# Kernel optimization log

Hardware: AMD Instinct MI355X
Metric: run time of the kernel (lower is better)

## Reference

```python
import jax, jax.numpy as jnp
import numpy as np

B, T, C = 32, 2048, 1024  # batch, seq_len (<= block_size), n_embd
HEAD_SIZE = 128


def setup_inputs() -> dict:
    key = jax.random.key(0)
    kx, kk, kq, kv = jax.random.split(key, 4)
    std = 0.02  # CustomLinear init: normal(0, 0.02)
    return {
        "x": jax.random.normal(kx, (B, T, C), dtype=jnp.float32),
        "Wk": jax.random.normal(kk, (HEAD_SIZE, C), dtype=jnp.float32) * std,
        "Wq": jax.random.normal(kq, (HEAD_SIZE, C), dtype=jnp.float32) * std,
        "Wv": jax.random.normal(kv, (HEAD_SIZE, C), dtype=jnp.float32) * std,
    }


def reference(x, Wk, Wq, Wv):
    # x: [B, T, C]; W*: [head_size, C] (torch Linear layout, no bias)
    Bb, Tt, Cc = x.shape
    k = jnp.einsum("btc,hc->bth", x, Wk)
    q = jnp.einsum("btc,hc->bth", x, Wq)
    v = jnp.einsum("btc,hc->bth", x, Wv)
    # NOTE: original scales by C**-0.5 (n_embd), not head_size**-0.5
    wei = jnp.einsum("bth,bsh->bts", q, k) * (Cc ** -0.5)
    causal = jnp.tril(jnp.ones((Tt, Tt), dtype=bool))  # tril[:T,:T]
    wei = jnp.where(causal, wei, -jnp.inf)
    wei = jax.nn.softmax(wei, axis=-1)
    return jnp.einsum("bts,bsh->bth", wei, v)  # [B, T, head_size]
```

## Files before the change

### kernel.cpp

```cpp
#include <hip/hip_runtime.h>
#include <hip/hip_bf16.h>

typedef __bf16 bf8_t __attribute__((ext_vector_type(8)));
typedef __bf16 bf4_t __attribute__((ext_vector_type(4)));
typedef float f4_t __attribute__((ext_vector_type(4)));

#define B_ 32
#define T_ 2048
#define C_ 1024
#define H_ 128

__global__ __launch_bounds__(256) void wconv_kernel(
    const float* __restrict__ Wk, const float* __restrict__ Wq, const float* __restrict__ Wv,
    __bf16* __restrict__ Wr)
{
    const int e  = (blockIdx.x * 256 + threadIdx.x) * 8;
    const int kk = e & 31;
    const int lr = (e >> 5) & 15;
    const int ks = (e >> 9) & 31;
    const int cg = e >> 14;
    const int col = cg * 16 + lr;
    const int k   = ks * 32 + kk;
    const float* W = (col < 128) ? Wk : (col < 256) ? Wq : Wv;
    const float* p = W + (size_t)(col & 127) * C_ + k;
    float4 f0 = *(const float4*)p;
    float4 f1 = *(const float4*)(p + 4);
    bf8_t o;
    o[0] = (__bf16)f0.x; o[1] = (__bf16)f0.y; o[2] = (__bf16)f0.z; o[3] = (__bf16)f0.w;
    o[4] = (__bf16)f1.x; o[5] = (__bf16)f1.y; o[6] = (__bf16)f1.z; o[7] = (__bf16)f1.w;
    *(bf8_t*)(Wr + e) = o;
}

__global__ __launch_bounds__(256, 1) void proj_kernel(
    const float* __restrict__ x, const __bf16* __restrict__ Wr,
    __bf16* __restrict__ Kb, __bf16* __restrict__ Qb, __bf16* __restrict__ VtG)
{
    __shared__ __bf16 Xs[64][C_ + 8];

    const int m0   = blockIdx.x * 64;
    const int tid  = threadIdx.x;
    const int lane = tid & 63;
    const int wn   = tid >> 6;
    const int lr   = lane & 15;
    const int quad = lane >> 4;
    const int r0   = tid >> 4;
    const int kc   = (tid & 15) << 3;

    f4_t acc[4][6];
    #pragma unroll
    for (int mi = 0; mi < 4; mi++)
        #pragma unroll
        for (int ni = 0; ni < 6; ni++) acc[mi][ni] = f4_t{0.f, 0.f, 0.f, 0.f};

    float4 bufA[8], bufB[8];

#define LOADC(buf, c) { _Pragma("unroll") \
    for (int i_ = 0; i_ < 4; ++i_) { \
        const float* p_ = x + (size_t)(m0 + r0 + i_ * 16) * C_ + (c) * 128 + kc; \
        buf[2 * i_]     = *(const float4*)p_; \
        buf[2 * i_ + 1] = *(const float4*)(p_ + 4); } }

#define WRITEC(buf, c) { _Pragma("unroll") \
    for (int i_ = 0; i_ < 4; ++i_) { \
        float4 a_ = buf[2 * i_], b_ = buf[2 * i_ + 1]; \
        bf8_t o_; \
        o_[0] = (__bf16)a_.x; o_[1] = (__bf16)a_.y; o_[2] = (__bf16)a_.z; o_[3] = (__bf16)a_.w; \
        o_[4] = (__bf16)b_.x; o_[5] = (__bf16)b_.y; o_[6] = (__bf16)b_.z; o_[7] = (__bf16)b_.w; \
        *(bf8_t*)&Xs[r0 + i_ * 16][(c) * 128 + kc] = o_; } }

#define COMPUTE(c) { _Pragma("unroll") \
    for (int k4_ = 0; k4_ < 4; ++k4_) { \
        const int ks_ = (c) * 4 + k4_; \
        bf8_t xa_[4]; \
        _Pragma("unroll") \
        for (int mi = 0; mi < 4; ++mi) \
            xa_[mi] = *(const bf8_t*)&Xs[mi * 16 + lr][ks_ * 32 + quad * 8]; \
        _Pragma("unroll") \
        for (int ni = 0; ni < 6; ++ni) { \
            bf8_t wb_ = *(const bf8_t*)(Wr + (size_t)((ni * 4 + wn) * 32 + ks_) * 512 + lr * 32 + quad * 8); \
            if (ni < 4) { \
                _Pragma("unroll") \
                for (int mi = 0; mi < 4; ++mi) \
                    acc[mi][ni] = __builtin_amdgcn_mfma_f32_16x16x32_bf16(xa_[mi], wb_, acc[mi][ni], 0, 0, 0); \
            } else { \
                _Pragma("unroll") \
                for (int mi = 0; mi < 4; ++mi) \
                    acc[mi][ni] = __builtin_amdgcn_mfma_f32_16x16x32_bf16(wb_, xa_[mi], acc[mi][ni], 0, 0, 0); \
            } } } }

    LOADC(bufA, 0)
    LOADC(bufB, 1)
    WRITEC(bufA, 0)
    __syncthreads();

    #pragma unroll
    for (int c = 0; c < 8; ++c) {
        if (c < 6) { if (c & 1) LOADC(bufB, c + 2) else LOADC(bufA, c + 2) }
        COMPUTE(c)
        if (c < 7) {
            if (c & 1) WRITEC(bufA, c + 1) else WRITEC(bufB, c + 1)
            __syncthreads();
        }
    }

#undef LOADC
#undef WRITEC
#undef COMPUTE

    const int bb = m0 >> 11;
    const int t0 = m0 & (T_ - 1);
    #pragma unroll
    for (int ni = 0; ni < 4; ni++) {
        __bf16* Out = (ni < 2) ? Kb : Qb;
        const int col = (ni & 1) * 64 + wn * 16 + lr;
        #pragma unroll
        for (int mi = 0; mi < 4; mi++)
            for (int r = 0; r < 4; r++) {
                const int row = m0 + mi * 16 + quad * 4 + r;
                Out[(size_t)row * H_ + col] = (__bf16)acc[mi][ni][r];
            }
    }
    #pragma unroll
    for (int ni = 4; ni < 6; ni++)
        for (int mi = 0; mi < 4; mi++) {
            const int tok = t0 + mi * 16 + lr;
            #pragma unroll
            for (int r = 0; r < 4; r++) {
                const int h = (ni - 4) * 64 + wn * 16 + quad * 4 + r;
                VtG[(size_t)bb * H_ * T_ + (size_t)h * T_ + tok] = (__bf16)acc[mi][ni][r];
            }
        }
}

__global__ __launch_bounds__(512, 4) void flash_kernel(
    const __bf16* __restrict__ Qb, const __bf16* __restrict__ Kb,
    const __bf16* __restrict__ VtG, float* __restrict__ Out)
{
    __shared__ __bf16 Ks[64][136];
    __shared__ __bf16 Vt[128][72];
    __shared__ __bf16 Ps[128][72];

    const int qt = (blockIdx.y < 16) ? (15 - blockIdx.x) : blockIdx.x;
    const int b  = blockIdx.y;
    const size_t kqbase = (size_t)b * T_ * H_;
    const size_t vbase  = (size_t)b * H_ * T_;

    const int tid  = threadIdx.x;
    const int lane = tid & 63;
    const int w    = tid >> 6;
    const int lr   = lane & 15;
    const int quad = lane >> 4;

    bf8_t qf[4];
    {
        const __bf16* qp = Qb + kqbase + (size_t)(qt * 128 + w * 16 + lr) * H_ + quad * 8;
        #pragma unroll
        for (int ks = 0; ks < 4; ks++) qf[ks] = *(const bf8_t*)(qp + ks * 32);
    }

    f4_t o[8];
    #pragma unroll
    for (int n = 0; n < 8; n++) o[n] = f4_t{0.f, 0.f, 0.f, 0.f};
    float ls[4] = {0.f, 0.f, 0.f, 0.f};

    const float sc = 0.03125f * 1.4426950408889634f;
    const int jmax = 2 * qt + 1;

    const int kRow0 = tid >> 4,          kC0 = (tid & 15) << 3;
    const int kRow1 = (tid + 512) >> 4,  kC1 = ((tid + 512) & 15) << 3;
    const int vH0 = tid >> 3,            vS0 = (tid & 7) << 3;
    const int vH1 = (tid + 512) >> 3,    vS1 = ((tid + 512) & 7) << 3;

    bf8_t kr0 = *(const bf8_t*)(Kb + kqbase + (size_t)kRow0 * H_ + kC0);
    bf8_t kr1 = *(const bf8_t*)(Kb + kqbase + (size_t)kRow1 * H_ + kC1);
    bf8_t vr0 = *(const bf8_t*)(VtG + vbase + (size_t)vH0 * T_ + vS0);
    bf8_t vr1 = *(const bf8_t*)(VtG + vbase + (size_t)vH1 * T_ + vS1);

    for (int j = 0; j <= jmax; j++) {
        __syncthreads();
        *(bf8_t*)&Ks[kRow0][kC0] = kr0;
        *(bf8_t*)&Ks[kRow1][kC1] = kr1;
        *(bf8_t*)&Vt[vH0][vS0]   = vr0;
        *(bf8_t*)&Vt[vH1][vS1]   = vr1;
        __syncthreads();
        if (j < jmax) {
            const int s0 = (j + 1) * 64;
            kr0 = *(const bf8_t*)(Kb + kqbase + (size_t)(s0 + kRow0) * H_ + kC0);
            kr1 = *(const bf8_t*)(Kb + kqbase + (size_t)(s0 + kRow1) * H_ + kC1);
            vr0 = *(const bf8_t*)(VtG + vbase + (size_t)vH0 * T_ + s0 + vS0);
            vr1 = *(const bf8_t*)(VtG + vbase + (size_t)vH1 * T_ + s0 + vS1);
        }
        if (j == jmax && w < 4) continue;

        f4_t s4[4];
        #pragma unroll
        for (int n = 0; n < 4; n++) s4[n] = f4_t{0.f, 0.f, 0.f, 0.f};
        #pragma unroll
        for (int ks = 0; ks < 4; ks++)
            for (int n = 0; n < 4; n++) {
                bf8_t kf = *(const bf8_t*)&Ks[n * 16 + lr][ks * 32 + quad * 8];
                s4[n] = __builtin_amdgcn_mfma_f32_16x16x32_bf16(qf[ks], kf, s4[n], 0, 0, 0);
            }

        const bool domask = (j - 2 * qt) == (w >> 2);
        const int rowg = qt * 128 + w * 16 + quad * 4;
        #pragma unroll
        for (int n = 0; n < 4; n++) {
            const int colg = j * 64 + n * 16 + lr;
            #pragma unroll
            for (int r = 0; r < 4; r++) {
                float p = __builtin_exp2f(s4[n][r] * sc);
                if (domask && colg > rowg + r) p = 0.f;
                ls[r] += p;
                Ps[w * 16 + quad * 4 + r][n * 16 + lr] = (__bf16)p;
            }
        }

        #pragma unroll
        for (int ks = 0; ks < 2; ks++) {
            bf8_t pf = *(const bf8_t*)&Ps[w * 16 + lr][ks * 32 + quad * 8];
            #pragma unroll
            for (int n = 0; n < 8; n++) {
                bf8_t vf = *(const bf8_t*)&Vt[n * 16 + lr][ks * 32 + quad * 8];
                o[n] = __builtin_amdgcn_mfma_f32_16x16x32_bf16(pf, vf, o[n], 0, 0, 0);
            }
        }
    }

    float inv[4];
    #pragma unroll
    for (int r = 0; r < 4; r++) {
        float v = ls[r];
        v += __shfl_xor(v, 1);
        v += __shfl_xor(v, 2);
        v += __shfl_xor(v, 4);
        v += __shfl_xor(v, 8);
        inv[r] = 1.f / v;
    }
    #pragma unroll
    for (int n = 0; n < 8; n++) {
        const int col = n * 16 + lr;
        #pragma unroll
        for (int r = 0; r < 4; r++) {
            const int row = qt * 128 + w * 16 + quad * 4 + r;
            Out[kqbase + (size_t)row * H_ + col] = o[n][r] * inv[r];
        }
    }
}

extern "C" void kernel_launch(void* const* d_in, const int* in_sizes, int n_in,
                              void* d_out, int out_size, void* d_ws, size_t ws_size,
                              hipStream_t stream) {
    const float* x  = (const float*)d_in[0];
    const float* Wk = (const float*)d_in[1];
    const float* Wq = (const float*)d_in[2];
    const float* Wv = (const float*)d_in[3];
    float* out = (float*)d_out;

    const size_t n_kqv = (size_t)B_ * T_ * H_;
    __bf16* Kb  = (__bf16*)d_ws;
    __bf16* Qb  = Kb + n_kqv;
    __bf16* VtG = Qb + n_kqv;
    __bf16* Wr  = VtG + n_kqv;

    wconv_kernel<<<dim3(192), 256, 0, stream>>>(Wk, Wq, Wv, Wr);
    proj_kernel<<<dim3((B_ * T_) / 64), 256, 0, stream>>>(x, Wr, Kb, Qb, VtG);
    flash_kernel<<<dim3(16, B_), 512, 0, stream>>>(Qb, Kb, VtG, out);
}
```

Baseline: 518.5 us.

## Shrink projection LDS tile to double-buffered 128-wide chunks, use 8 waves per block

The projection kernel used to stage a full 64x1024 bf16 tile of x in shared memory (about 130 KB), which allowed only one block per CU. It now double-buffers 64x128 chunks (about 35 KB) and uses 512 threads, with the waves split 2x4 over rows and columns. Each wave holds half the accumulators, and launch bounds are raised to allow 4 blocks per CU. The aim is higher occupancy and better latency hiding for the x loads. In exchange, each Wr fragment is loaded by twice as many waves, and the prefetch is only one chunk ahead.

```diff
diff --git a/kernel.cpp b/kernel.cpp
--- a/kernel.cpp
+++ b/kernel.cpp
@@ -31,74 +31,71 @@
     *(bf8_t*)(Wr + e) = o;
 }
 
-__global__ __launch_bounds__(256, 1) void proj_kernel(
+__global__ __launch_bounds__(512, 4) void proj_kernel(
     const float* __restrict__ x, const __bf16* __restrict__ Wr,
     __bf16* __restrict__ Kb, __bf16* __restrict__ Qb, __bf16* __restrict__ VtG)
 {
-    __shared__ __bf16 Xs[64][C_ + 8];
+    __shared__ __bf16 Xs[2][64][136];
 
     const int m0   = blockIdx.x * 64;
     const int tid  = threadIdx.x;
     const int lane = tid & 63;
-    const int wn   = tid >> 6;
+    const int w    = tid >> 6;
+    const int wm   = w >> 2;
+    const int wn   = w & 3;
     const int lr   = lane & 15;
     const int quad = lane >> 4;
-    const int r0   = tid >> 4;
-    const int kc   = (tid & 15) << 3;
-
-    f4_t acc[4][6];
-    #pragma unroll
-    for (int mi = 0; mi < 4; mi++)
+
+    const int r0 = tid >> 5;
+    const int c4 = (tid & 31) << 2;
+
+    f4_t acc[2][6];
+    #pragma unroll
+    for (int mi = 0; mi < 2; mi++)
         #pragma unroll
         for (int ni = 0; ni < 6; ni++) acc[mi][ni] = f4_t{0.f, 0.f, 0.f, 0.f};
 
-    float4 bufA[8], bufB[8];
-
-#define LOADC(buf, c) { _Pragma("unroll") \
+    float4 pf[4];
+
+#define LOADC(c) { _Pragma("unroll") \
+    for (int i_ = 0; i_ < 4; ++i_) \
+        pf[i_] = *(const float4*)(x + (size_t)(m0 + r0 + i_ * 16) * C_ + (c) * 128 + c4); }
+
+#define WRITEC(bsel) { _Pragma("unroll") \
     for (int i_ = 0; i_ < 4; ++i_) { \
-        const float* p_ = x + (size_t)(m0 + r0 + i_ * 16) * C_ + (c) * 128 + kc; \
-        buf[2 * i_]     = *(const float4*)p_; \
-        buf[2 * i_ + 1] = *(const float4*)(p_ + 4); } }
-
-#define WRITEC(buf, c) { _Pragma("unroll") \
-    for (int i_ = 0; i_ < 4; ++i_) { \
-        float4 a_ = buf[2 * i_], b_ = buf[2 * i_ + 1]; \
-        bf8_t o_; \
-        o_[0] = (__bf16)a_.x; o_[1] = (__bf16)a_.y; o_[2] = (__bf16)a_.z; o_[3] = (__bf16)a_.w; \
-        o_[4] = (__bf16)b_.x; o_[5] = (__bf16)b_.y; o_[6] = (__bf16)b_.z; o_[7] = (__bf16)b_.w; \
-        *(bf8_t*)&Xs[r0 + i_ * 16][(c) * 128 + kc] = o_; } }
-
-#define COMPUTE(c) { _Pragma("unroll") \
+        float4 f_ = pf[i_]; \
+        *(bf4_t*)&Xs[bsel][r0 + i_ * 16][c4] = \
+            bf4_t{(__bf16)f_.x, (__bf16)f_.y, (__bf16)f_.z, (__bf16)f_.w}; } }
+
+#define COMPUTE(c, bsel) { _Pragma("unroll") \
     for (int k4_ = 0; k4_ < 4; ++k4_) { \
-        const int ks_ = (c) * 4 + k4_; \
-        bf8_t xa_[4]; \
+        bf8_t xa_[2]; \
         _Pragma("unroll") \
-        for (int mi = 0; mi < 4; ++mi) \
-            xa_[mi] = *(const bf8_t*)&Xs[mi * 16 + lr][ks_ * 32 + quad * 8]; \
+        for (int mi = 0; mi < 2; ++mi) \
+            xa_[mi] = *(const bf8_t*)&Xs[bsel][wm * 32 + mi * 16 + lr][k4_ * 32 + quad * 8]; \
         _Pragma("unroll") \
         for (int ni = 0; ni < 6; ++ni) { \
-            bf8_t wb_ = *(const bf8_t*)(Wr + (size_t)((ni * 4 + wn) * 32 + ks_) * 512 + lr * 32 + quad * 8); \
+            bf8_t wb_ = *(const bf8_t*)(Wr + (size_t)((ni * 4 + wn) * 32 + (c) * 4 + k4_) * 512 + lr * 32 + quad * 8); \
             if (ni < 4) { \
                 _Pragma("unroll") \
-                for (int mi = 0; mi < 4; ++mi) \
+                for (int mi = 0; mi < 2; ++mi) \
                     acc[mi][ni] = __builtin_amdgcn_mfma_f32_16x16x32_bf16(xa_[mi], wb_, acc[mi][ni], 0, 0, 0); \
             } else { \
                 _Pragma("unroll") \
-                for (int mi = 0; mi < 4; ++mi) \
+                for (int mi = 0; mi < 2; ++mi) \
                     acc[mi][ni] = __builtin_amdgcn_mfma_f32_16x16x32_bf16(wb_, xa_[mi], acc[mi][ni], 0, 0, 0); \
             } } } }
 
-    LOADC(bufA, 0)
-    LOADC(bufB, 1)
-    WRITEC(bufA, 0)
+    LOADC(0)
+    WRITEC(0)
     __syncthreads();
 
     #pragma unroll
     for (int c = 0; c < 8; ++c) {
-        if (c < 6) { if (c & 1) LOADC(bufB, c + 2) else LOADC(bufA, c + 2) }
-        COMPUTE(c)
+        if (c < 7) LOADC(c + 1)
+        COMPUTE(c, c & 1)
         if (c < 7) {
-            if (c & 1) WRITEC(bufA, c + 1) else WRITEC(bufB, c + 1)
+            WRITEC((c + 1) & 1)
             __syncthreads();
         }
     }
@@ -114,16 +111,16 @@
         __bf16* Out = (ni < 2) ? Kb : Qb;
         const int col = (ni & 1) * 64 + wn * 16 + lr;
         #pragma unroll
-        for (int mi = 0; mi < 4; mi++)
+        for (int mi = 0; mi < 2; mi++)
             for (int r = 0; r < 4; r++) {
-                const int row = m0 + mi * 16 + quad * 4 + r;
+                const int row = m0 + wm * 32 + mi * 16 + quad * 4 + r;
                 Out[(size_t)row * H_ + col] = (__bf16)acc[mi][ni][r];
             }
     }
     #pragma unroll
     for (int ni = 4; ni < 6; ni++)
-        for (int mi = 0; mi < 4; mi++) {
-            const int tok = t0 + mi * 16 + lr;
+        for (int mi = 0; mi < 2; mi++) {
+            const int tok = t0 + wm * 32 + mi * 16 + lr;
             #pragma unroll
             for (int r = 0; r < 4; r++) {
                 const int h = (ni - 4) * 64 + wn * 16 + quad * 4 + r;
@@ -264,6 +261,6 @@
     __bf16* Wr  = VtG + n_kqv;
 
     wconv_kernel<<<dim3(192), 256, 0, stream>>>(Wk, Wq, Wv, Wr);
-    proj_kernel<<<dim3((B_ * T_) / 64), 256, 0, stream>>>(x, Wr, Kb, Qb, VtG);
+    proj_kernel<<<dim3((B_ * T_) / 64), 512, 0, stream>>>(x, Wr, Kb, Qb, VtG);
     flash_kernel<<<dim3(16, B_), 512, 0, stream>>>(Qb, Kb, VtG, out);
 }
```

New measurement: 511.3 us. Within noise of the previous version (-1.4%).
